# Optimization experiments

Hardware: AMD Instinct MI355X
Metric: run time of the kernel (lower is better)

The kernel has to match this reference:

```python
import jax, jax.numpy as jnp
import numpy as np

C_IN = 2048
C_HID = 1024
C_EMB = 256


def setup_inputs() -> dict:
    key = jax.random.key(0)
    ks = jax.random.split(key, 14)
    B, T = 4, 2048
    sc = 0.02  # keep logits in a sane range for softmax
    inp = {
        "x": jax.random.normal(ks[0], (B, T, C_IN), jnp.float32) * 0.05,
        "theta_w": jax.random.normal(ks[1], (C_HID, C_IN), jnp.float32) * sc,
        "theta_b": jnp.zeros((C_HID,), jnp.float32),
        "phi_w": jax.random.normal(ks[2], (C_HID, C_IN), jnp.float32) * sc,
        "phi_b": jnp.zeros((C_HID,), jnp.float32),
        "g_w": jax.random.normal(ks[3], (C_HID, C_IN), jnp.float32) * sc,
        "g_b": jnp.zeros((C_HID,), jnp.float32),
        "rou_w": jax.random.normal(ks[4], (2,), jnp.float32),
        "rou_b": jnp.zeros((1,), jnp.float32),
        "w_w": jax.random.normal(ks[5], (C_IN, C_HID), jnp.float32) * sc,
        "w_b": jnp.zeros((C_IN,), jnp.float32),
        "emb_w": jax.random.normal(ks[6], (C_EMB, C_IN), jnp.float32) * sc,
        "emb_b": jnp.zeros((C_EMB,), jnp.float32),
        "B": B,
        "T": T,
    }
    return inp


def reference(x, theta_w, theta_b, phi_w, phi_b, g_w, g_b, rou_w, rou_b,
              w_w, w_b, emb_w, emb_b, B, T):
    x = x.reshape(B, T, C_IN)
    # NSSM: raw self-similarity + softmax over last dim -> (B, T, T)
    nssm = jax.nn.softmax(jnp.einsum('btc,bsc->bts', x, x), axis=-1)
    xc = jnp.swapaxes(x, 1, 2)  # (B, C_IN, T), channels-first like Conv1d
    # 1x1 Conv1d == per-timestep linear over channels
    x_theta = jnp.einsum('oc,bct->bot', theta_w, xc) + theta_b[None, :, None]  # (B,H,T)
    x_phi = jnp.einsum('oc,bct->bto', phi_w, xc) + phi_b[None, None, :]        # (B,T,H)
    att = jax.nn.softmax(jnp.einsum('bth,bhs->bts', x_phi, x_theta), axis=-1)  # (B,T,T)
    # Faithful to torch.cat(dim=0).view(B,-1,T,T): row-major interleave of batches
    cat = jnp.concatenate([nssm, att], axis=0).reshape(B, 2, T, T)
    # rou: 1x1 Conv2d(2->1) == weighted sum of the two maps + bias, then softmax
    moca = jax.nn.softmax(rou_w[0] * cat[:, 0] + rou_w[1] * cat[:, 1] + rou_b[0], axis=-1)  # (B,T,T)
    x_g = jnp.einsum('oc,bct->bot', g_w, xc) + g_b[None, :, None]  # (B,H,T)
    y = jnp.einsum('bht,bts->bhs', x_g, moca)                      # (B,H,T)
    wz = jnp.einsum('oh,bht->bot', w_w, y) + w_b[None, :, None]    # (B,C_IN,T)
    z = jnp.swapaxes(wz + xc, 1, 2)                                # (B,T,C_IN)
    return z @ emb_w.T + emb_b                                     # (B,T,256)
```

## Files before the change

kernel.cpp:

```cpp
#include <hip/hip_runtime.h>
#include <hip/hip_bf16.h>

constexpr int kB   = 4;
constexpr int kT   = 2048;
constexpr int kCIN = 2048;
constexpr int kHID = 1024;
constexpr int kEMB = 256;

typedef __bf16 bf16_t;
typedef __bf16 bf16x8 __attribute__((ext_vector_type(8)));
typedef __bf16 bf16x4 __attribute__((ext_vector_type(4)));
typedef float  f32x4  __attribute__((ext_vector_type(4)));

__device__ __forceinline__ void gll16(const void* g, void* l) {
  auto lp = reinterpret_cast<__attribute__((address_space(3))) uint32_t*>(
      reinterpret_cast<uintptr_t>(l));
  __builtin_amdgcn_global_load_lds(static_cast<const uint32_t*>(g), lp, 16, 0, 0);
}

#define MFMA_BF16 __builtin_amdgcn_mfma_f32_16x16x32_bf16

template <int MODE>
__device__ __forceinline__ void gemm256(bf16_t* lds, const bf16_t* A, const bf16_t* B,
                                        void* Cv, int lda, int ldb, int ldc,
                                        int m0, int n0, int Klen, const float* biasN) {
  const int tid  = threadIdx.x;
  const int lane = tid & 63, wv = tid >> 6;
  const int wm = wv & 1, wn = wv >> 1;
  const int lm = lane & 15, q = lane >> 4;
  const int l8 = lane >> 3;
  const int slot = (lane & 7) ^ l8;

  bf16_t* const sA = lds;
  bf16_t* const sB = lds + 32768;

  int aoff[4], boff[4];
#pragma unroll
  for (int cc = 0; cc < 4; cc++) {
    const int ra = cc * 64 + wv * 8 + l8;
    aoff[cc] = ra * lda;
    const int nb = ((ra >> 5) & 3) * 64 + (ra >> 7) * 32 + (ra & 31);
    boff[cc] = nb * ldb;
  }
  const bf16_t* const Ab = A + (size_t)m0 * lda + slot * 8;
  const bf16_t* const Bb = B + (size_t)n0 * ldb + slot * 8;

  const int x0 = ((q ^ (lm & 7)) << 3);
  const int x1 = (((q + 4) ^ (lm & 7)) << 3);

#define STAGE_A(T, H)                                                         \
  {                                                                           \
    bf16_t* dst_ = sA + (((T) & 1) << 14);                                    \
    const bf16_t* src_ = Ab + ((T) << 6);                                     \
    gll16(src_ + aoff[(H)], dst_ + ((H) << 12) + (wv << 9));                  \
    gll16(src_ + aoff[2 + (H)], dst_ + ((2 + (H)) << 12) + (wv << 9));        \
  }
#define STAGE_B(T, G)                                                         \
  {                                                                           \
    bf16_t* dst_ = sB + (((T) & 1) << 14);                                    \
    const bf16_t* src_ = Bb + ((T) << 6);                                     \
    gll16(src_ + boff[2 * (G)], dst_ + ((2 * (G)) << 12) + (wv << 9));        \
    gll16(src_ + boff[2 * (G) + 1], dst_ + ((2 * (G) + 1) << 12) + (wv << 9));\
  }
#define READ_A(BUF, H)                                                        \
  _Pragma("unroll") for (int i = 0; i < 4; i++) {                             \
    const bf16_t* p_ = (BUF) + ((wm * 128 + (H) * 64 + i * 16 + lm) << 6);    \
    af[i][0] = *(const bf16x8*)(p_ + x0);                                     \
    af[i][1] = *(const bf16x8*)(p_ + x1);                                     \
  }
#define READ_B(BF, BUF, G)                                                    \
  _Pragma("unroll") for (int j2 = 0; j2 < 2; j2++) {                          \
    const bf16_t* p_ = (BUF) + (((G) * 128 + wn * 32 + j2 * 16 + lm) << 6);   \
    BF[j2][0] = *(const bf16x8*)(p_ + x0);                                    \
    BF[j2][1] = *(const bf16x8*)(p_ + x1);                                    \
  }
#define QUAD(H, G, BF)                                                        \
  _Pragma("unroll") for (int i2 = 0; i2 < 4; i2++)                            \
  _Pragma("unroll") for (int j2 = 0; j2 < 2; j2++)                            \
  _Pragma("unroll") for (int kk = 0; kk < 2; kk++)                            \
    acc[(H) * 4 + i2][(G) * 2 + j2] = MFMA_BF16(                              \
        af[i2][kk], BF[j2][kk], acc[(H) * 4 + i2][(G) * 2 + j2], 0, 0, 0);
#define MFMA_OPEN()                                                           \
  asm volatile("s_waitcnt lgkmcnt(0)" ::: "memory");                          \
  __builtin_amdgcn_s_setprio(1);
#define MFMA_CLOSE() __builtin_amdgcn_s_setprio(0);

  f32x4 acc[8][4];
#pragma unroll
  for (int i = 0; i < 8; i++)
#pragma unroll
    for (int j = 0; j < 4; j++)
#pragma unroll
      for (int r = 0; r < 4; r++) acc[i][j][r] = 0.f;

  const int nt = Klen >> 6;

  STAGE_A(0, 0) STAGE_B(0, 0) STAGE_B(0, 1) STAGE_A(0, 1)
  STAGE_A(1, 0) STAGE_B(1, 0) STAGE_B(1, 1) STAGE_A(1, 1)
  asm volatile("s_waitcnt vmcnt(8)" ::: "memory");
  __builtin_amdgcn_s_barrier();

  bf16x8 af[4][2], bf0[2][2], bf1[2][2];
  for (int t = 0; t < nt; t++) {
    bf16_t* const a = sA + ((t & 1) << 14);
    bf16_t* const b = sB + ((t & 1) << 14);
    const bool pf = (t + 2) < nt;
    READ_A(a, 0)
    READ_B(bf0, b, 0)
    asm volatile("s_waitcnt lgkmcnt(8)" ::: "memory");
    __builtin_amdgcn_s_barrier();
    MFMA_OPEN()
    QUAD(0, 0, bf0)
    MFMA_CLOSE()
    __builtin_amdgcn_s_barrier();
    READ_B(bf1, b, 1)
    if (pf) STAGE_A(t + 2, 0)
    __builtin_amdgcn_s_barrier();
    MFMA_OPEN()
    QUAD(0, 1, bf1)
    MFMA_CLOSE()
    __builtin_amdgcn_s_barrier();
    READ_A(a, 1)
    if (pf) STAGE_B(t + 2, 0)
    __builtin_amdgcn_s_barrier();
    MFMA_OPEN()
    QUAD(1, 1, bf1)
    MFMA_CLOSE()
    __builtin_amdgcn_s_barrier();
    if (pf) { STAGE_B(t + 2, 1) STAGE_A(t + 2, 1) }
    __builtin_amdgcn_s_barrier();
    __builtin_amdgcn_s_setprio(1);
    QUAD(1, 0, bf0)
    __builtin_amdgcn_s_setprio(0);
    if (pf)
      asm volatile("s_waitcnt vmcnt(8)" ::: "memory");
    else if (t + 1 < nt)
      asm volatile("s_waitcnt vmcnt(0)" ::: "memory");
    __builtin_amdgcn_s_barrier();
  }

#pragma unroll
  for (int i = 0; i < 8; i++) {
    const int gm = m0 + wm * 128 + (i >> 2) * 64 + (i & 3) * 16 + q * 4;
#pragma unroll
    for (int j = 0; j < 4; j++) {
      const int gn = n0 + wn * 64 + j * 16 + lm;
      const float bn_ = biasN ? biasN[gn] : 0.f;
#pragma unroll
      for (int r = 0; r < 4; r++) {
        const float v = acc[i][j][r] + bn_;
        const size_t idx = (size_t)(gm + r) * ldc + gn;
        if (MODE == 0) ((bf16_t*)Cv)[idx] = (bf16_t)v;
        else           atomicAdd(&((float*)Cv)[idx], v);
      }
    }
  }
#undef STAGE_A
#undef STAGE_B
#undef READ_A
#undef READ_B
#undef QUAD
#undef MFMA_OPEN
#undef MFMA_CLOSE
}

__global__ __launch_bounds__(256) void k_prep(const float* __restrict__ x,
                                              const float* __restrict__ th,
                                              const float* __restrict__ ph,
                                              const float* __restrict__ g,
                                              const float* __restrict__ emb,
                                              const float* __restrict__ w_w,
                                              const float* __restrict__ w_b,
                                              const float* __restrict__ emb_b,
                                              const float* __restrict__ tb,
                                              const float* __restrict__ pb,
                                              const float* __restrict__ gb,
                                              bf16_t* __restrict__ xbf,
                                              bf16_t* __restrict__ wqkv,
                                              bf16_t* __restrict__ embbf,
                                              bf16_t* __restrict__ wwT,
                                              float* __restrict__ biase,
                                              float* __restrict__ bqkv,
                                              float* __restrict__ out) {
  __shared__ float tile[64 * 66];
  const int b = blockIdx.x;
  if (b < 23040) {
    const float* in; bf16_t* o; long i;
    if (b < 16384)      { in = x;   o = xbf;                            i = (long)b * 256 + threadIdx.x; }
    else if (b < 18432) { in = th;  o = wqkv;                           i = (long)(b - 16384) * 256 + threadIdx.x; }
    else if (b < 20480) { in = ph;  o = wqkv + (size_t)kHID * kCIN;     i = (long)(b - 18432) * 256 + threadIdx.x; }
    else if (b < 22528) { in = g;   o = wqkv + (size_t)2 * kHID * kCIN; i = (long)(b - 20480) * 256 + threadIdx.x; }
    else                { in = emb; o = embbf;                          i = (long)(b - 22528) * 256 + threadIdx.x; }
    float4 v = ((const float4*)in)[i];
    bf16x4 ov;
    ov[0] = (bf16_t)v.x; ov[1] = (bf16_t)v.y; ov[2] = (bf16_t)v.z; ov[3] = (bf16_t)v.w;
    ((bf16x4*)o)[i] = ov;
  } else if (b < 23552) {
    int j = b - 23040;
    int h0 = (j & 15) * 64, c0 = (j >> 4) * 64;
#pragma unroll
    for (int k = 0; k < 16; k++) {
      int e = k * 256 + threadIdx.x;
      int r = e >> 6, c = e & 63;
      tile[r * 66 + c] = w_w[(size_t)(c0 + r) * kHID + h0 + c];
    }
    __syncthreads();
#pragma unroll
    for (int k = 0; k < 16; k++) {
      int e = k * 256 + threadIdx.x;
      int r = e >> 6, c = e & 63;
      wwT[(size_t)(h0 + r) * kCIN + c0 + c] = (bf16_t)tile[c * 66 + r];
    }
  } else if (b < 23808) {
    int e = b - 23552;
    float acc = 0.f;
    for (int c = threadIdx.x; c < kCIN; c += 256)
      acc += emb[(size_t)e * kCIN + c] * w_b[c];
#pragma unroll
    for (int o = 32; o > 0; o >>= 1) acc += __shfl_xor(acc, o, 64);
    __syncthreads();
    if ((threadIdx.x & 63) == 0) tile[threadIdx.x >> 6] = acc;
    __syncthreads();
    if (threadIdx.x == 0) biase[e] = tile[0] + tile[1] + tile[2] + tile[3] + emb_b[e];
  } else if (b < 23820) {
    int i = (b - 23808) * 256 + threadIdx.x;
    if (i < 3072)
      bqkv[i] = i < 1024 ? tb[i] : (i < 2048 ? pb[i - 1024] : gb[i - 2048]);
  } else {
    long i = (long)(b - 23820) * 256 + threadIdx.x;
    ((float4*)out)[i] = make_float4(0.f, 0.f, 0.f, 0.f);
  }
}

__global__ __launch_bounds__(512, 2) void k_mega1(const bf16_t* __restrict__ xbf,
                                                  const bf16_t* __restrict__ wqkv,
                                                  const bf16_t* __restrict__ embbf,
                                                  const bf16_t* __restrict__ wwT,
                                                  bf16_t* __restrict__ xtphi,
                                                  bf16_t* __restrict__ S1,
                                                  bf16_t* __restrict__ Mbf,
                                                  const float* __restrict__ bqkv) {
  __shared__ bf16_t lds[65536];
  const int tile = blockIdx.x;
  if (tile < 384) {
    const int bm = tile & 31, bn = tile >> 5;
    gemm256<0>(lds, xbf, wqkv, xtphi, 2048, 2048, 3072,
               bm * 256, bn * 256, 2048, bqkv);
  } else if (tile < 528) {
    int s = tile - 384;
    const int z = s / 36;
    int tt = s % 36, rr = 0;
    while (tt >= 8 - rr) { tt -= 8 - rr; rr++; }
    const bf16_t* Az = xbf + (size_t)z * kT * kCIN;
    gemm256<0>(lds, Az, Az, S1 + (size_t)z * kT * kT, 2048, 2048, 2048,
               rr * 256, (rr + tt) * 256, 2048, nullptr);
  } else {
    const int m = tile - 528;
    gemm256<0>(lds, embbf, wwT, Mbf, 2048, 2048, 1024, 0, m * 256, 2048, nullptr);
  }
}

__global__ __launch_bounds__(512, 2) void k_gemm2(const bf16_t* __restrict__ xtphi,
                                                  bf16_t* __restrict__ S2) {
  __shared__ bf16_t lds[65536];
  const int bid = blockIdx.x;
  const int bm = bid & 7, bn = (bid >> 3) & 7, z = bid >> 6;
  const bf16_t* base = xtphi + (size_t)z * kT * 3072;
  gemm256<0>(lds, base + 1024, base, S2 + (size_t)z * kT * kT, 3072, 3072, 2048,
             bm * 256, bn * 256, 1024, nullptr);
}

__global__ __launch_bounds__(256) void k_util(bf16_t* __restrict__ S1,
                                              const bf16_t* __restrict__ xtphi,
                                              bf16_t* __restrict__ xgT) {
  __shared__ bf16_t tile[64 * 66];
  const int bid = blockIdx.x;
  const size_t T2 = (size_t)kT * kT;
  if (bid < 1984) {
    int z = bid / 496, t = bid % 496, qq = 0;
    while (t >= 31 - qq) { t -= 31 - qq; qq++; }
    int p = qq + 1 + t;
    const size_t base = (size_t)z * T2;
#pragma unroll
    for (int k = 0; k < 16; k++) {
      int e = k * 256 + threadIdx.x;
      int r = e >> 6, c = e & 63;
      tile[r * 66 + c] = S1[base + (size_t)(qq * 64 + r) * kT + p * 64 + c];
    }
    __syncthreads();
#pragma unroll
    for (int k = 0; k < 16; k++) {
      int e = k * 256 + threadIdx.x;
      int r = e >> 6, c = e & 63;
      S1[base + (size_t)(p * 64 + r) * kT + qq * 64 + c] = tile[c * 66 + r];
    }
  } else {
    int j = bid - 1984;
    int hb = j & 15, tb2 = (j >> 4) & 31, z = j >> 9;
#pragma unroll
    for (int k = 0; k < 16; k++) {
      int e = k * 256 + threadIdx.x;
      int r = e >> 6, c = e & 63;
      tile[r * 66 + c] = xtphi[(size_t)(z * kT + tb2 * 64 + r) * 3072 + 2048 + hb * 64 + c];
    }
    __syncthreads();
#pragma unroll
    for (int k = 0; k < 16; k++) {
      int e = k * 256 + threadIdx.x;
      int r = e >> 6, c = e & 63;
      xgT[(size_t)z * kHID * kT + (size_t)(hb * 64 + r) * kT + tb2 * 64 + c] = tile[c * 66 + r];
    }
  }
}

__global__ __launch_bounds__(256) void k_moca(const bf16_t* __restrict__ S1,
                                              const bf16_t* __restrict__ S2,
                                              bf16_t* __restrict__ dst,
                                              const float* __restrict__ rou_w,
                                              const float* __restrict__ rou_b) {
  __shared__ float s[4];
  const int t = blockIdx.x, b = blockIdx.y;
  const size_t T2 = (size_t)kT * kT;
  const bf16_t* src = (b < 2) ? S1 : S2;
  const int pb = (b < 2) ? 2 * b : 2 * (b - 2);
  const bf16_t* rA = src + (size_t)pb * T2 + (size_t)t * kT;
  const bf16_t* rB = rA + T2;
  const int base = threadIdx.x * 8;

  float va[8], vb[8];
  {
    bf16x8 a = *(const bf16x8*)(rA + base);
    bf16x8 bb = *(const bf16x8*)(rB + base);
#pragma unroll
    for (int j = 0; j < 8; j++) { va[j] = (float)a[j]; vb[j] = (float)bb[j]; }
  }
  auto red_max = [&](float v) {
#pragma unroll
    for (int o = 32; o > 0; o >>= 1) v = fmaxf(v, __shfl_xor(v, o, 64));
    __syncthreads();
    if ((threadIdx.x & 63) == 0) s[threadIdx.x >> 6] = v;
    __syncthreads();
    return fmaxf(fmaxf(s[0], s[1]), fmaxf(s[2], s[3]));
  };
  auto red_sum = [&](float v) {
#pragma unroll
    for (int o = 32; o > 0; o >>= 1) v += __shfl_xor(v, o, 64);
    __syncthreads();
    if ((threadIdx.x & 63) == 0) s[threadIdx.x >> 6] = v;
    __syncthreads();
    return (s[0] + s[1]) + (s[2] + s[3]);
  };

  float m = -1e30f, acc;
#pragma unroll
  for (int j = 0; j < 8; j++) m = fmaxf(m, va[j]);
  m = red_max(m); acc = 0.f;
#pragma unroll
  for (int j = 0; j < 8; j++) { va[j] = __expf(va[j] - m); acc += va[j]; }
  float invA = 1.f / red_sum(acc);

  m = -1e30f;
#pragma unroll
  for (int j = 0; j < 8; j++) m = fmaxf(m, vb[j]);
  m = red_max(m); acc = 0.f;
#pragma unroll
  for (int j = 0; j < 8; j++) { vb[j] = __expf(vb[j] - m); acc += vb[j]; }
  float invB = 1.f / red_sum(acc);

  const float r0 = rou_w[0], r1 = rou_w[1], rb = rou_b[0];
#pragma unroll
  for (int j = 0; j < 8; j++) va[j] = r0 * va[j] * invA + r1 * vb[j] * invB + rb;

  m = -1e30f;
#pragma unroll
  for (int j = 0; j < 8; j++) m = fmaxf(m, va[j]);
  m = red_max(m); acc = 0.f;
#pragma unroll
  for (int j = 0; j < 8; j++) { va[j] = __expf(va[j] - m); acc += va[j]; }
  float invC = 1.f / red_sum(acc);

  bf16x8 o;
#pragma unroll
  for (int j = 0; j < 8; j++) o[j] = (bf16_t)(va[j] * invC);
  *(bf16x8*)(dst + (size_t)b * T2 + (size_t)t * kT + base) = o;
}

__global__ __launch_bounds__(256) void k_mocaT(const bf16_t* __restrict__ in,
                                               bf16_t* __restrict__ out) {
  __shared__ bf16_t tile[64 * 66];
  size_t base = (size_t)blockIdx.z * kT * kT;
  int r0 = blockIdx.y * 64, c0 = blockIdx.x * 64;
#pragma unroll
  for (int k = 0; k < 16; k++) {
    int e = k * 256 + threadIdx.x;
    int r = e >> 6, c = e & 63;
    tile[r * 66 + c] = in[base + (size_t)(r0 + r) * kT + c0 + c];
  }
  __syncthreads();
#pragma unroll
  for (int k = 0; k < 16; k++) {
    int e = k * 256 + threadIdx.x;
    int r = e >> 6, c = e & 63;
    out[base + (size_t)(c0 + r) * kT + r0 + c] = tile[c * 66 + r];
  }
}

__global__ __launch_bounds__(512, 2) void k_tail1(const bf16_t* __restrict__ mocaT,
                                                  const bf16_t* __restrict__ xgT,
                                                  bf16_t* __restrict__ yT,
                                                  const bf16_t* __restrict__ xbf,
                                                  const bf16_t* __restrict__ embbf,
                                                  float* __restrict__ out,
                                                  const float* __restrict__ biase) {
  __shared__ bf16_t lds[65536];
  const int bid = blockIdx.x;
  if (bid < 128) {
    const int bm = bid & 7, bn = (bid >> 3) & 3, z = bid >> 5;
    gemm256<0>(lds, mocaT + (size_t)z * kT * kT, xgT + (size_t)z * kHID * kT,
               yT + (size_t)z * kT * kHID, 2048, 2048, 1024,
               bm * 256, bn * 256, 2048, nullptr);
  } else {
    const int r = bid - 128;
    const int bm = r & 31, ks = r >> 5;
    gemm256<2>(lds, xbf + ks * 512, embbf + ks * 512, out, 2048, 2048, 256,
               bm * 256, 0, 512, ks == 0 ? biase : nullptr);
  }
}

__global__ __launch_bounds__(512, 2) void k_tail2(const bf16_t* __restrict__ yT,
                                                  const bf16_t* __restrict__ Mbf,
                                                  float* __restrict__ out) {
  __shared__ bf16_t lds[65536];
  const int bid = blockIdx.x;
  const int bm = bid & 31, ks = bid >> 5;
  gemm256<2>(lds, yT + ks * 256, Mbf + ks * 256, out, 1024, 1024, 256,
             bm * 256, 0, 256, nullptr);
}

extern "C" void kernel_launch(void* const* d_in, const int* in_sizes, int n_in,
                              void* d_out, int out_size, void* d_ws, size_t ws_size,
                              hipStream_t stream) {
  const float* x       = (const float*)d_in[0];
  const float* theta_w = (const float*)d_in[1];
  const float* theta_b = (const float*)d_in[2];
  const float* phi_w   = (const float*)d_in[3];
  const float* phi_b   = (const float*)d_in[4];
  const float* g_w     = (const float*)d_in[5];
  const float* g_b     = (const float*)d_in[6];
  const float* rou_w   = (const float*)d_in[7];
  const float* rou_b   = (const float*)d_in[8];
  const float* w_w     = (const float*)d_in[9];
  const float* w_b     = (const float*)d_in[10];
  const float* emb_w   = (const float*)d_in[11];
  const float* emb_b   = (const float*)d_in[12];
  float* out = (float*)d_out;

  char* ws = (char*)d_ws;
  size_t off = 0;
  auto alloc = [&](size_t bytes) -> char* {
    off = (off + 255) & ~(size_t)255;
    char* p = ws + off;
    off += bytes;
    return p;
  };

  const size_t BT = (size_t)kB * kT;
  const size_t T2 = (size_t)kT * kT;

  bf16_t* xbf   = (bf16_t*)alloc(BT * kCIN * 2);
  bf16_t* wqkv  = (bf16_t*)alloc((size_t)3 * kHID * kCIN * 2);
  bf16_t* embbf = (bf16_t*)alloc((size_t)kEMB * kCIN * 2);
  bf16_t* wwT   = (bf16_t*)alloc((size_t)kHID * kCIN * 2);
  bf16_t* xtphi = (bf16_t*)alloc(BT * 3072 * 2);
  bf16_t* xgT   = (bf16_t*)alloc((size_t)kB * kHID * kT * 2);
  bf16_t* mocab = (bf16_t*)alloc((size_t)kB * T2 * 2);
  bf16_t* Mbf   = (bf16_t*)alloc((size_t)kEMB * kHID * 2);
  float*  biase = (float*)alloc((size_t)kEMB * 4);
  float*  bqkv  = (float*)alloc((size_t)3072 * 4);
  bf16_t* S1    = (bf16_t*)alloc((size_t)kB * T2 * 2);
  bf16_t* S2    = (bf16_t*)alloc((size_t)kB * T2 * 2);
  bf16_t* mocaT = (bf16_t*)xtphi;
  bf16_t* yT    = (bf16_t*)S2;

  k_prep<<<dim3(25868), 256, 0, stream>>>(x, theta_w, phi_w, g_w, emb_w, w_w, w_b,
                                          emb_b, theta_b, phi_b, g_b,
                                          xbf, wqkv, embbf, wwT, biase, bqkv, out);
  k_mega1<<<dim3(532), 512, 0, stream>>>(xbf, wqkv, embbf, wwT, xtphi, S1, Mbf, bqkv);
  k_gemm2<<<dim3(256), 512, 0, stream>>>(xtphi, S2);
  k_util<<<dim3(4032), 256, 0, stream>>>(S1, xtphi, xgT);
  k_moca<<<dim3(kT, kB), 256, 0, stream>>>(S1, S2, mocab, rou_w, rou_b);
  k_mocaT<<<dim3(32, 32, kB), 256, 0, stream>>>(mocab, mocaT);
  k_tail1<<<dim3(256), 512, 0, stream>>>(mocaT, xgT, yT, xbf, embbf, out, biase);
  k_tail2<<<dim3(128), 512, 0, stream>>>(yT, Mbf, out);
}
```

Before: 493.0 us.

## Restructure GEMM main loop scheduling and add XCD-aware block swizzle

The 256x256 GEMM inner loop is reorganized from four barrier-separated MFMA quadrants into two halves. Each half issues its LDS reads up front, and the global prefetch stages are grouped between the halves, which removes several barriers and explicit lgkmcnt waits per iteration. A block-index swizzle is also added so that consecutive tiles land on the same XCD, aiming for better L2 reuse in the mega1 and gemm2 kernels. With fewer explicit waits, the code relies on compiler-inserted waitcnts, and the overlap between LDS reads and global loads into LDS may change.

```diff
diff --git a/kernel.cpp b/kernel.cpp
--- a/kernel.cpp
+++ b/kernel.cpp
@@ -80,10 +80,6 @@
   _Pragma("unroll") for (int kk = 0; kk < 2; kk++)                            \
     acc[(H) * 4 + i2][(G) * 2 + j2] = MFMA_BF16(                              \
         af[i2][kk], BF[j2][kk], acc[(H) * 4 + i2][(G) * 2 + j2], 0, 0, 0);
-#define MFMA_OPEN()                                                           \
-  asm volatile("s_waitcnt lgkmcnt(0)" ::: "memory");                          \
-  __builtin_amdgcn_s_setprio(1);
-#define MFMA_CLOSE() __builtin_amdgcn_s_setprio(0);
 
   f32x4 acc[8][4];
 #pragma unroll
@@ -107,35 +103,25 @@
     const bool pf = (t + 2) < nt;
     READ_A(a, 0)
     READ_B(bf0, b, 0)
-    asm volatile("s_waitcnt lgkmcnt(8)" ::: "memory");
+    READ_B(bf1, b, 1)
+    __builtin_amdgcn_s_setprio(1);
+    QUAD(0, 0, bf0)
+    QUAD(0, 1, bf1)
+    __builtin_amdgcn_s_setprio(0);
     __builtin_amdgcn_s_barrier();
-    MFMA_OPEN()
-    QUAD(0, 0, bf0)
-    MFMA_CLOSE()
-    __builtin_amdgcn_s_barrier();
-    READ_B(bf1, b, 1)
-    if (pf) STAGE_A(t + 2, 0)
-    __builtin_amdgcn_s_barrier();
-    MFMA_OPEN()
-    QUAD(0, 1, bf1)
-    MFMA_CLOSE()
-    __builtin_amdgcn_s_barrier();
+    if (pf) { STAGE_A(t + 2, 0) STAGE_B(t + 2, 0) STAGE_B(t + 2, 1) }
     READ_A(a, 1)
-    if (pf) STAGE_B(t + 2, 0)
-    __builtin_amdgcn_s_barrier();
-    MFMA_OPEN()
+    __builtin_amdgcn_s_setprio(1);
     QUAD(1, 1, bf1)
-    MFMA_CLOSE()
-    __builtin_amdgcn_s_barrier();
-    if (pf) { STAGE_B(t + 2, 1) STAGE_A(t + 2, 1) }
-    __builtin_amdgcn_s_barrier();
-    __builtin_amdgcn_s_setprio(1);
     QUAD(1, 0, bf0)
     __builtin_amdgcn_s_setprio(0);
-    if (pf)
+    __builtin_amdgcn_s_barrier();
+    if (pf) {
+      STAGE_A(t + 2, 1)
       asm volatile("s_waitcnt vmcnt(8)" ::: "memory");
-    else if (t + 1 < nt)
+    } else if (t + 1 < nt) {
       asm volatile("s_waitcnt vmcnt(0)" ::: "memory");
+    }
     __builtin_amdgcn_s_barrier();
   }
 
@@ -160,8 +146,12 @@
 #undef READ_A
 #undef READ_B
 #undef QUAD
-#undef MFMA_OPEN
-#undef MFMA_CLOSE
+}
+
+__device__ __forceinline__ int xcd_swz(int bid, int nwg) {
+  const int qq = nwg >> 3, rr = nwg & 7;
+  const int xcd = bid & 7, idx = bid >> 3;
+  return (xcd < rr ? xcd * (qq + 1) : rr * (qq + 1) + (xcd - rr) * qq) + idx;
 }
 
 __global__ __launch_bounds__(256) void k_prep(const float* __restrict__ x,
@@ -241,7 +231,7 @@
                                                   bf16_t* __restrict__ Mbf,
                                                   const float* __restrict__ bqkv) {
   __shared__ bf16_t lds[65536];
-  const int tile = blockIdx.x;
+  const int tile = xcd_swz(blockIdx.x, 532);
   if (tile < 384) {
     const int bm = tile & 31, bn = tile >> 5;
     gemm256<0>(lds, xbf, wqkv, xtphi, 2048, 2048, 3072,
@@ -263,7 +253,7 @@
 __global__ __launch_bounds__(512, 2) void k_gemm2(const bf16_t* __restrict__ xtphi,
                                                   bf16_t* __restrict__ S2) {
   __shared__ bf16_t lds[65536];
-  const int bid = blockIdx.x;
+  const int bid = xcd_swz(blockIdx.x, 256);
   const int bm = bid & 7, bn = (bid >> 3) & 7, z = bid >> 6;
   const bf16_t* base = xtphi + (size_t)z * kT * 3072;
   gemm256<0>(lds, base + 1024, base, S2 + (size_t)z * kT * kT, 3072, 3072, 2048,
```

After: 488.9 us. No clear change (-0.8%).
